# Optimization experiments

Measured on AMD Instinct MI355X. Metric: run time of the kernel, lower is better.

## Reference

```python
import jax, jax.numpy as jnp
import numpy as np

D = 1024
H = 16
F = 4096
EPS = 1e-6


def _layernorm(x, alpha, bias):
    # Faithful to torch: unbiased std (ddof=1), divide by (std + eps)
    mean = jnp.mean(x, axis=-1, keepdims=True)
    std = jnp.std(x, axis=-1, keepdims=True, ddof=1)
    return alpha * (x - mean) / (std + EPS) + bias


def setup_inputs() -> dict:
    key = jax.random.key(0)
    ks = jax.random.split(key, 12)
    B, S = 2, 2048
    s = 1.0 / np.sqrt(D)
    inp = {
        "x": jax.random.normal(ks[0], (B, S, D), jnp.float32),
        "mask": jnp.ones((B, 1, 1, S), jnp.int32),
        "wq": jax.random.normal(ks[1], (D, D), jnp.float32) * s,
        "bq": jnp.zeros((D,), jnp.float32),
        "wk": jax.random.normal(ks[2], (D, D), jnp.float32) * s,
        "bk": jnp.zeros((D,), jnp.float32),
        "wv": jax.random.normal(ks[3], (D, D), jnp.float32) * s,
        "bv": jnp.zeros((D,), jnp.float32),
        "wo": jax.random.normal(ks[4], (D, D), jnp.float32) * s,
        "bo": jnp.zeros((D,), jnp.float32),
        "ln1_a": jnp.ones((D,), jnp.float32),
        "ln1_b": jnp.zeros((D,), jnp.float32),
        "ln2_a": jnp.ones((D,), jnp.float32),
        "ln2_b": jnp.zeros((D,), jnp.float32),
        "w1": jax.random.normal(ks[5], (D, F), jnp.float32) * s,
        "b1": jnp.zeros((F,), jnp.float32),
        "w2": jax.random.normal(ks[6], (F, D), jnp.float32) * (1.0 / np.sqrt(F)),
        "b2": jnp.zeros((D,), jnp.float32),
    }
    return inp


def reference(x, mask, wq, bq, wk, bk, wv, bv, wo, bo,
              ln1_a, ln1_b, ln2_a, ln2_b, w1, b1, w2, b2):
    B, S, _ = x.shape
    dk = D // H
    # --- residual 1: pre-LN self-attention ---
    h = _layernorm(x, ln1_a, ln1_b)
    q = (h @ wq + bq).reshape(B, S, H, dk).transpose(0, 2, 1, 3)
    k = (h @ wk + bk).reshape(B, S, H, dk).transpose(0, 2, 1, 3)
    v = (h @ wv + bv).reshape(B, S, H, dk).transpose(0, 2, 1, 3)
    scores = jnp.einsum('bhqd,bhkd->bhqk', q, k) / jnp.sqrt(jnp.float32(dk))
    scores = jnp.where(mask == 0, jnp.float32(-1e9), scores)
    attn = jax.nn.softmax(scores, axis=-1)
    ctx = jnp.einsum('bhqk,bhkd->bhqd', attn, v)
    ctx = ctx.transpose(0, 2, 1, 3).reshape(B, S, D)
    x = x + (ctx @ wo + bo)
    # --- residual 2: pre-LN feed-forward ---
    h = _layernorm(x, ln2_a, ln2_b)
    ff = jax.nn.relu(h @ w1 + b1) @ w2 + b2
    return x + ff
```

## Files before the change

kernel.cpp:

```cpp
#include <hip/hip_runtime.h>
#include <hip/hip_bf16.h>

typedef __attribute__((ext_vector_type(8))) short bf16x8;
typedef __attribute__((ext_vector_type(4))) float f32x4;
typedef unsigned int uint32;

#define DMODEL 1024
#define SEQ    2048
#define NB     2
#define NH     16
#define HD     64
#define FDIM   4096
#define NTOK   (NB*SEQ)

__device__ __forceinline__ void async16(const void* g, void* s) {
    __builtin_amdgcn_global_load_lds((const __attribute__((address_space(1))) unsigned int*)g,
                                     (__attribute__((address_space(3))) unsigned int*)s,
                                     16, 0, 0);
}

__global__ __launch_bounds__(256) void transpose_cvt_k(const float* __restrict__ src,
                                                       __hip_bfloat16* __restrict__ dst,
                                                       int R, int C) {
    __shared__ __hip_bfloat16 tile[32][33];
    int tx = threadIdx.x, ty = threadIdx.y;
    int bx = blockIdx.x * 32, by = blockIdx.y * 32;
    for (int i = 0; i < 32; i += 8)
        tile[ty + i][tx] = __float2bfloat16(src[(size_t)(by + ty + i) * C + bx + tx]);
    __syncthreads();
    for (int i = 0; i < 32; i += 8)
        dst[(size_t)(bx + ty + i) * R + by + tx] = tile[tx][ty + i];
}

__global__ __launch_bounds__(256) void ln_kernel(const float* __restrict__ x,
                                                 const float* __restrict__ alpha,
                                                 const float* __restrict__ beta,
                                                 __hip_bfloat16* __restrict__ out) {
    const int row = blockIdx.x, tid = threadIdx.x;
    const size_t base = (size_t)row * DMODEL;
    float v[4];
    for (int e = 0; e < 4; ++e) v[e] = x[base + tid * 4 + e];
    float s1 = v[0] + v[1] + v[2] + v[3];
    float s2 = v[0]*v[0] + v[1]*v[1] + v[2]*v[2] + v[3]*v[3];
    for (int off = 32; off > 0; off >>= 1) {
        s1 += __shfl_down(s1, off);
        s2 += __shfl_down(s2, off);
    }
    __shared__ float red[8];
    int w = tid >> 6, lane = tid & 63;
    if (lane == 0) { red[w * 2] = s1; red[w * 2 + 1] = s2; }
    __syncthreads();
    if (tid == 0) {
        float a = 0.f, b = 0.f;
        for (int i = 0; i < 4; ++i) { a += red[2 * i]; b += red[2 * i + 1]; }
        red[0] = a; red[1] = b;
    }
    __syncthreads();
    s1 = red[0]; s2 = red[1];
    float mean = s1 * (1.0f / DMODEL);
    float var  = fmaxf((s2 - (float)DMODEL * mean * mean) * (1.0f / (DMODEL - 1)), 0.f);
    float inv  = 1.0f / (sqrtf(var) + 1e-6f);
    for (int e = 0; e < 4; ++e) {
        int c = tid * 4 + e;
        float y = alpha[c] * (v[e] - mean) * inv + beta[c];
        out[base + c] = __float2bfloat16(y);
    }
}

template <int EPI>
__global__ __launch_bounds__(256) void gemm_bt(const __hip_bfloat16* __restrict__ A,
                                               const __hip_bfloat16* __restrict__ Bt,
                                               const float* __restrict__ bias,
                                               const float* __restrict__ res,
                                               void* __restrict__ Cout,
                                               int M, int N, int K) {
    __shared__ alignas(16) __hip_bfloat16 As[2][128 * 32];
    __shared__ alignas(16) __hip_bfloat16 Bs[2][128 * 32];
    const int tid = threadIdx.x, l = tid & 63;
    const int w = tid >> 6;
    const int wm = w >> 1, wn = w & 1, quad = l >> 4, lc = l & 15;
    const int row0 = blockIdx.y * 128, col0 = blockIdx.x * 128;
    const int srow = 32 * w + (l >> 2), scol = (l & 3) * 8;

    f32x4 acc[4][4];
    for (int i = 0; i < 4; ++i)
        for (int j = 0; j < 4; ++j) acc[i][j] = (f32x4){0.f, 0.f, 0.f, 0.f};

    for (int c = 0; c < 2; ++c) {
        async16(A  + (size_t)(row0 + srow + 16 * c) * K + scol, (char*)&As[0][0] + w * 2048 + c * 1024);
        async16(Bt + (size_t)(col0 + srow + 16 * c) * K + scol, (char*)&Bs[0][0] + w * 2048 + c * 1024);
    }
    const int NKT = K / 32;
    for (int kt = 0; kt < NKT; ++kt) {
        const int cur = kt & 1;
        __syncthreads();
        if (kt + 1 < NKT) {
            const int k1 = (kt + 1) * 32;
            for (int c = 0; c < 2; ++c) {
                async16(A  + (size_t)(row0 + srow + 16 * c) * K + k1 + scol, (char*)&As[cur ^ 1][0] + w * 2048 + c * 1024);
                async16(Bt + (size_t)(col0 + srow + 16 * c) * K + k1 + scol, (char*)&Bs[cur ^ 1][0] + w * 2048 + c * 1024);
            }
        }
        bf16x8 af[4], bfr[4];
        for (int i = 0; i < 4; ++i) af[i]  = *(const bf16x8*)&As[cur][(64 * wm + 16 * i + lc) * 32 + quad * 8];
        for (int j = 0; j < 4; ++j) bfr[j] = *(const bf16x8*)&Bs[cur][(64 * wn + 16 * j + lc) * 32 + quad * 8];
        for (int i = 0; i < 4; ++i)
            for (int j = 0; j < 4; ++j)
                acc[i][j] = __builtin_amdgcn_mfma_f32_16x16x32_bf16(af[i], bfr[j], acc[i][j], 0, 0, 0);
    }

    __hip_bfloat16* Cb = (__hip_bfloat16*)Cout;
    float* Cf = (float*)Cout;
    for (int j = 0; j < 4; ++j) {
        int col = col0 + 64 * wn + 16 * j + lc;
        float bv = bias[col];
        for (int i = 0; i < 4; ++i) {
            int rbase = row0 + 64 * wm + 16 * i + quad * 4;
            for (int r = 0; r < 4; ++r) {
                size_t idx = (size_t)(rbase + r) * N + col;
                float vacc = acc[i][j][r] + bv;
                if (EPI == 0)      Cb[idx] = __float2bfloat16(vacc);
                else if (EPI == 1) Cb[idx] = __float2bfloat16(fmaxf(vacc, 0.f));
                else               Cf[idx] = vacc + res[idx];
            }
        }
    }
}

__global__ __launch_bounds__(256) void gemm_qkv(const __hip_bfloat16* __restrict__ A,
                                                const __hip_bfloat16* __restrict__ Bt,
                                                const float* __restrict__ bq,
                                                const float* __restrict__ bk,
                                                const float* __restrict__ bv,
                                                __hip_bfloat16* __restrict__ qout,
                                                __hip_bfloat16* __restrict__ kout,
                                                __hip_bfloat16* __restrict__ vTout) {
    const int K = DMODEL;
    __shared__ alignas(16) __hip_bfloat16 As[2][128 * 32];
    __shared__ alignas(16) __hip_bfloat16 Bs[2][128 * 32];
    const int tid = threadIdx.x, l = tid & 63;
    const int w = tid >> 6;
    const int wm = w >> 1, wn = w & 1, quad = l >> 4, lc = l & 15;
    const int row0 = blockIdx.y * 128, col0 = blockIdx.x * 128;
    const int srow = 32 * w + (l >> 2), scol = (l & 3) * 8;

    f32x4 acc[4][4];
    for (int i = 0; i < 4; ++i)
        for (int j = 0; j < 4; ++j) acc[i][j] = (f32x4){0.f, 0.f, 0.f, 0.f};

    for (int c = 0; c < 2; ++c) {
        async16(A  + (size_t)(row0 + srow + 16 * c) * K + scol, (char*)&As[0][0] + w * 2048 + c * 1024);
        async16(Bt + (size_t)(col0 + srow + 16 * c) * K + scol, (char*)&Bs[0][0] + w * 2048 + c * 1024);
    }
    const int NKT = K / 32;
    for (int kt = 0; kt < NKT; ++kt) {
        const int cur = kt & 1;
        __syncthreads();
        if (kt + 1 < NKT) {
            const int k1 = (kt + 1) * 32;
            for (int c = 0; c < 2; ++c) {
                async16(A  + (size_t)(row0 + srow + 16 * c) * K + k1 + scol, (char*)&As[cur ^ 1][0] + w * 2048 + c * 1024);
                async16(Bt + (size_t)(col0 + srow + 16 * c) * K + k1 + scol, (char*)&Bs[cur ^ 1][0] + w * 2048 + c * 1024);
            }
        }
        bf16x8 af[4], bfr[4];
        for (int i = 0; i < 4; ++i) af[i]  = *(const bf16x8*)&As[cur][(64 * wm + 16 * i + lc) * 32 + quad * 8];
        for (int j = 0; j < 4; ++j) bfr[j] = *(const bf16x8*)&Bs[cur][(64 * wn + 16 * j + lc) * 32 + quad * 8];
        for (int i = 0; i < 4; ++i)
            for (int j = 0; j < 4; ++j)
                acc[i][j] = __builtin_amdgcn_mfma_f32_16x16x32_bf16(af[i], bfr[j], acc[i][j], 0, 0, 0);
    }

    const int seg = col0 >> 10;
    const float* bias = (seg == 0) ? bq : (seg == 1) ? bk : bv;
    for (int j = 0; j < 4; ++j) {
        int col  = col0 + 64 * wn + 16 * j + lc;
        int colm = col & (DMODEL - 1);
        float bvx = bias[colm];
        for (int i = 0; i < 4; ++i) {
            int rbase = row0 + 64 * wm + 16 * i + quad * 4;
            for (int r = 0; r < 4; ++r) {
                int trow = rbase + r;
                float vacc = acc[i][j][r] + bvx;
                if (seg == 2) {
                    int bb = trow >> 11, s = trow & (SEQ - 1);
                    int hh = colm >> 6, d = colm & (HD - 1);
                    vTout[((size_t)(bb * NH + hh) * HD + d) * SEQ + s] = __float2bfloat16(vacc);
                } else {
                    __hip_bfloat16* dst = (seg == 0) ? qout : kout;
                    dst[(size_t)trow * DMODEL + colm] = __float2bfloat16(vacc);
                }
            }
        }
    }
}

__global__ __launch_bounds__(256) void attn_kernel(const __hip_bfloat16* __restrict__ q,
                                                   const __hip_bfloat16* __restrict__ k,
                                                   const __hip_bfloat16* __restrict__ vT,
                                                   const int* __restrict__ mask,
                                                   __hip_bfloat16* __restrict__ ctx) {
    const int qt = blockIdx.x, bh = blockIdx.y;
    const int b = bh >> 4;
    const int q0 = qt * 128;
    const int tid = threadIdx.x, w = tid >> 6, l = tid & 63, quad = l >> 4, lc = l & 15;

    __shared__ alignas(16) __hip_bfloat16 Kh[2][2][64 * 32];
    __shared__ alignas(16) __hip_bfloat16 Vh[2][2][64 * 32];
    __shared__ uint32 Ps32[4][16 * 33];

    const size_t base   = (size_t)b * SEQ * DMODEL + (size_t)(bh & 15) * HD;
    const size_t vtbase = (size_t)bh * HD * SEQ;

    bf16x8 qf[2][2];
    for (int s = 0; s < 2; ++s) {
        const __hip_bfloat16* qrow = &q[base + (size_t)(q0 + s * 64 + w * 16 + lc) * DMODEL];
        qf[s][0] = *(const bf16x8*)&qrow[quad * 8];
        qf[s][1] = *(const bf16x8*)&qrow[32 + quad * 8];
    }

    f32x4 o[2][4];
    for (int s = 0; s < 2; ++s)
        for (int dj = 0; dj < 4; ++dj) o[s][dj] = (f32x4){0.f, 0.f, 0.f, 0.f};
    float rsp[2][4] = {{0.f,0.f,0.f,0.f},{0.f,0.f,0.f,0.f}};

    const int lr = l >> 2, lc8 = (l & 3) * 8;

    for (int c = 0; c < 2; ++c) {
        const int W = w * 2 + c;
        const int rr = (W & 3) * 16 + lr, cc8 = (W >> 2) * 32 + lc8;
        async16(&k [base   + (size_t)rr * DMODEL + cc8], (char*)&Kh[0][0][0] + W * 1024);
        async16(&vT[vtbase + (size_t)rr * SEQ + cc8],    (char*)&Vh[0][0][0] + W * 1024);
    }

    const int NT = SEQ / 64;
    for (int kt = 0; kt < NT; ++kt) {
        const int k0 = kt * 64;
        const int cur = kt & 1;

        __syncthreads();
        if (kt + 1 < NT) {
            const int k1 = k0 + 64;
            for (int c = 0; c < 2; ++c) {
                const int W = w * 2 + c;
                const int rr = (W & 3) * 16 + lr, cc8 = (W >> 2) * 32 + lc8;
                async16(&k [base   + (size_t)(k1 + rr) * DMODEL + cc8], (char*)&Kh[cur ^ 1][0][0] + W * 1024);
                async16(&vT[vtbase + (size_t)rr * SEQ + k1 + cc8],      (char*)&Vh[cur ^ 1][0][0] + W * 1024);
            }
        }
        int mc[4];
        for (int jn = 0; jn < 4; ++jn) mc[jn] = mask[b * SEQ + k0 + jn * 16 + lc];

        bf16x8 kf0[4], kf1[4];
        for (int jn = 0; jn < 4; ++jn) {
            kf0[jn] = *(const bf16x8*)&Kh[cur][0][(jn * 16 + lc) * 32 + quad * 8];
            kf1[jn] = *(const bf16x8*)&Kh[cur][1][(jn * 16 + lc) * 32 + quad * 8];
        }
        f32x4 sa[2][4];
        for (int s = 0; s < 2; ++s)
            for (int jn = 0; jn < 4; ++jn) {
                f32x4 z = (f32x4){0.f, 0.f, 0.f, 0.f};
                z = __builtin_amdgcn_mfma_f32_16x16x32_bf16(qf[s][0], kf0[jn], z, 0, 0, 0);
                z = __builtin_amdgcn_mfma_f32_16x16x32_bf16(qf[s][1], kf1[jn], z, 0, 0, 0);
                sa[s][jn] = z;
            }

        bf16x8 vf0[4], vf1[4];
        for (int dj = 0; dj < 4; ++dj) {
            vf0[dj] = *(const bf16x8*)&Vh[cur][0][(dj * 16 + lc) * 32 + quad * 8];
            vf1[dj] = *(const bf16x8*)&Vh[cur][1][(dj * 16 + lc) * 32 + quad * 8];
        }

        for (int s = 0; s < 2; ++s) {
            float p[4][4];
            for (int jn = 0; jn < 4; ++jn)
                for (int r = 0; r < 4; ++r)
                    p[jn][r] = mc[jn] ? __expf(sa[s][jn][r] * 0.125f) : 0.f;
            for (int r = 0; r < 4; ++r)
                rsp[s][r] += (p[0][r] + p[1][r]) + (p[2][r] + p[3][r]);

            volatile unsigned short* psw = (volatile unsigned short*)&Ps32[w][0];
            for (int jn = 0; jn < 4; ++jn)
                for (int r = 0; r < 4; ++r) {
                    __hip_bfloat16 hb = __float2bfloat16(p[jn][r]);
                    psw[(quad * 4 + r) * 66 + jn * 16 + lc] = *(unsigned short*)&hb;
                }
            volatile uint32* plr = (volatile uint32*)&Ps32[w][0];
            union { uint32 u[4]; bf16x8 v8; } pf0, pf1;
            for (int j = 0; j < 4; ++j) {
                pf0.u[j] = plr[lc * 33 + quad * 4 + j];
                pf1.u[j] = plr[lc * 33 + 16 + quad * 4 + j];
            }
            for (int dj = 0; dj < 4; ++dj) {
                o[s][dj] = __builtin_amdgcn_mfma_f32_16x16x32_bf16(pf0.v8, vf0[dj], o[s][dj], 0, 0, 0);
                o[s][dj] = __builtin_amdgcn_mfma_f32_16x16x32_bf16(pf1.v8, vf1[dj], o[s][dj], 0, 0, 0);
            }
        }
    }

    for (int s = 0; s < 2; ++s) {
        for (int r = 0; r < 4; ++r) {
            float rs = rsp[s][r];
            for (int off = 1; off < 16; off <<= 1) rs += __shfl_xor(rs, off, 16);
            float linv = 1.0f / rs;
            int row = q0 + s * 64 + w * 16 + quad * 4 + r;
            for (int dj = 0; dj < 4; ++dj)
                ctx[base + (size_t)row * DMODEL + dj * 16 + lc] = __float2bfloat16(o[s][dj][r] * linv);
        }
    }
}

extern "C" void kernel_launch(void* const* d_in, const int* in_sizes, int n_in,
                              void* d_out, int out_size, void* d_ws, size_t ws_size,
                              hipStream_t stream) {
    const float* x    = (const float*)d_in[0];
    const int*   mask = (const int*)d_in[1];
    const float* wq = (const float*)d_in[2];
    const float* bq = (const float*)d_in[3];
    const float* wk = (const float*)d_in[4];
    const float* bk = (const float*)d_in[5];
    const float* wv = (const float*)d_in[6];
    const float* bv = (const float*)d_in[7];
    const float* wo = (const float*)d_in[8];
    const float* bo = (const float*)d_in[9];
    const float* ln1_a = (const float*)d_in[10];
    const float* ln1_b = (const float*)d_in[11];
    const float* ln2_a = (const float*)d_in[12];
    const float* ln2_b = (const float*)d_in[13];
    const float* w1 = (const float*)d_in[14];
    const float* b1 = (const float*)d_in[15];
    const float* w2 = (const float*)d_in[16];
    const float* b2 = (const float*)d_in[17];
    float* out = (float*)d_out;

    char* ws = (char*)d_ws;
    const size_t SZ_WT  = (size_t)DMODEL * DMODEL * 2;
    const size_t SZ_ACT = (size_t)NTOK * DMODEL * 2;
    const size_t SZ_WF  = (size_t)FDIM * DMODEL * 2;
    size_t off = 0;
    __hip_bfloat16* wqkvT = (__hip_bfloat16*)(ws + off); off += 3 * SZ_WT;
    __hip_bfloat16* woT   = (__hip_bfloat16*)(ws + off); off += SZ_WT;
    __hip_bfloat16* w1T   = (__hip_bfloat16*)(ws + off); off += SZ_WF;
    __hip_bfloat16* w2T   = (__hip_bfloat16*)(ws + off); off += SZ_WF;
    __hip_bfloat16* h1    = (__hip_bfloat16*)(ws + off); off += SZ_ACT;
    __hip_bfloat16* qb    = (__hip_bfloat16*)(ws + off); off += SZ_ACT;
    __hip_bfloat16* kb    = (__hip_bfloat16*)(ws + off); off += SZ_ACT;
    __hip_bfloat16* vTb   = (__hip_bfloat16*)(ws + off); off += SZ_ACT;
    __hip_bfloat16* ctx   = (__hip_bfloat16*)(ws + off); off += SZ_ACT;
    float*          x1    = (float*)(ws + off);          off += (size_t)NTOK * DMODEL * 4;
    __hip_bfloat16* h2    = (__hip_bfloat16*)(ws + off); off += SZ_ACT;
    __hip_bfloat16* ff1   = h1;

    dim3 tb(32, 8);
    transpose_cvt_k<<<dim3(32, 32), tb, 0, stream>>>(wq, wqkvT,                   DMODEL, DMODEL);
    transpose_cvt_k<<<dim3(32, 32), tb, 0, stream>>>(wk, wqkvT + 1024 * DMODEL,   DMODEL, DMODEL);
    transpose_cvt_k<<<dim3(32, 32), tb, 0, stream>>>(wv, wqkvT + 2048 * DMODEL,   DMODEL, DMODEL);
    transpose_cvt_k<<<dim3(32, 32), tb, 0, stream>>>(wo, woT, DMODEL, DMODEL);
    transpose_cvt_k<<<dim3(128, 32), tb, 0, stream>>>(w1, w1T, DMODEL, FDIM);
    transpose_cvt_k<<<dim3(32, 128), tb, 0, stream>>>(w2, w2T, FDIM, DMODEL);

    ln_kernel<<<NTOK, 256, 0, stream>>>(x, ln1_a, ln1_b, h1);

    gemm_qkv<<<dim3(3 * DMODEL / 128, NTOK / 128), 256, 0, stream>>>(h1, wqkvT, bq, bk, bv, qb, kb, vTb);

    attn_kernel<<<dim3(SEQ / 128, NB * NH), 256, 0, stream>>>(qb, kb, vTb, mask, ctx);

    gemm_bt<2><<<dim3(DMODEL / 128, NTOK / 128), 256, 0, stream>>>(ctx, woT, bo, x, x1, NTOK, DMODEL, DMODEL);

    ln_kernel<<<NTOK, 256, 0, stream>>>(x1, ln2_a, ln2_b, h2);

    gemm_bt<1><<<dim3(FDIM / 128, NTOK / 128), 256, 0, stream>>>(h2, w1T, b1, nullptr, ff1, NTOK, FDIM, DMODEL);
    gemm_bt<2><<<dim3(DMODEL / 128, NTOK / 128), 256, 0, stream>>>(ff1, w2T, b2, x1, out, NTOK, DMODEL, FDIM);
}
```

Before: 453.8 us.

## Swizzle K/V LDS tiles and pass P via lane shuffles instead of LDS

The attention kernel now computes S transposed (K as the A operand), so each lane holds the scores for one query column across four key rows. It packs the probabilities to bf16 and rearranges them into the PV MFMA operand layout with two xor-shuffles, which removes the per-wave LDS scratch round trip for P. K/V tiles are written to and read from LDS with an XOR swizzle to reduce bank conflicts, mask loads are vectorized to int4, and s_setprio is raised around the MFMA blocks. The row-sum reduction is reworked to match the new layout, which adds shuffle and select work and depends on the lane-mapping being correct.

```diff
diff --git a/kernel.cpp b/kernel.cpp
--- a/kernel.cpp
+++ b/kernel.cpp
@@ -207,7 +207,6 @@
 
     __shared__ alignas(16) __hip_bfloat16 Kh[2][2][64 * 32];
     __shared__ alignas(16) __hip_bfloat16 Vh[2][2][64 * 32];
-    __shared__ uint32 Ps32[4][16 * 33];
 
     const size_t base   = (size_t)b * SEQ * DMODEL + (size_t)(bh & 15) * HD;
     const size_t vtbase = (size_t)bh * HD * SEQ;
@@ -222,13 +221,16 @@
     f32x4 o[2][4];
     for (int s = 0; s < 2; ++s)
         for (int dj = 0; dj < 4; ++dj) o[s][dj] = (f32x4){0.f, 0.f, 0.f, 0.f};
-    float rsp[2][4] = {{0.f,0.f,0.f,0.f},{0.f,0.f,0.f,0.f}};
-
-    const int lr = l >> 2, lc8 = (l & 3) * 8;
+    float rsp2[2] = {0.f, 0.f};
+
+    const int lr  = l >> 2, cb = l & 3;
+    const int cbsw = ((cb ^ ((lr >> 1) & 3))) * 8;
+    const int rsw  = (lc >> 1) & 3;
+    const int b1v = (l >> 5) & 1, b0v = (l >> 4) & 1;
 
     for (int c = 0; c < 2; ++c) {
         const int W = w * 2 + c;
-        const int rr = (W & 3) * 16 + lr, cc8 = (W >> 2) * 32 + lc8;
+        const int rr = (W & 3) * 16 + lr, cc8 = (W >> 2) * 32 + cbsw;
         async16(&k [base   + (size_t)rr * DMODEL + cc8], (char*)&Kh[0][0][0] + W * 1024);
         async16(&vT[vtbase + (size_t)rr * SEQ + cc8],    (char*)&Vh[0][0][0] + W * 1024);
     }
@@ -243,66 +245,91 @@
             const int k1 = k0 + 64;
             for (int c = 0; c < 2; ++c) {
                 const int W = w * 2 + c;
-                const int rr = (W & 3) * 16 + lr, cc8 = (W >> 2) * 32 + lc8;
+                const int rr = (W & 3) * 16 + lr, cc8 = (W >> 2) * 32 + cbsw;
                 async16(&k [base   + (size_t)(k1 + rr) * DMODEL + cc8], (char*)&Kh[cur ^ 1][0][0] + W * 1024);
                 async16(&vT[vtbase + (size_t)rr * SEQ + k1 + cc8],      (char*)&Vh[cur ^ 1][0][0] + W * 1024);
             }
         }
-        int mc[4];
-        for (int jn = 0; jn < 4; ++jn) mc[jn] = mask[b * SEQ + k0 + jn * 16 + lc];
+        int4 mc[4];
+        for (int jn = 0; jn < 4; ++jn)
+            mc[jn] = *(const int4*)&mask[b * SEQ + k0 + jn * 16 + quad * 4];
 
         bf16x8 kf0[4], kf1[4];
         for (int jn = 0; jn < 4; ++jn) {
-            kf0[jn] = *(const bf16x8*)&Kh[cur][0][(jn * 16 + lc) * 32 + quad * 8];
-            kf1[jn] = *(const bf16x8*)&Kh[cur][1][(jn * 16 + lc) * 32 + quad * 8];
-        }
-        f32x4 sa[2][4];
-        for (int s = 0; s < 2; ++s)
+            kf0[jn] = *(const bf16x8*)&Kh[cur][0][(jn * 16 + lc) * 32 + (quad ^ rsw) * 8];
+            kf1[jn] = *(const bf16x8*)&Kh[cur][1][(jn * 16 + lc) * 32 + (quad ^ rsw) * 8];
+        }
+        bf16x8 vf0[4], vf1[4];
+        for (int dj = 0; dj < 4; ++dj) {
+            vf0[dj] = *(const bf16x8*)&Vh[cur][0][(dj * 16 + lc) * 32 + (quad ^ rsw) * 8];
+            vf1[dj] = *(const bf16x8*)&Vh[cur][1][(dj * 16 + lc) * 32 + (quad ^ rsw) * 8];
+        }
+
+        for (int s = 0; s < 2; ++s) {
+            f32x4 sa[4];
+            __builtin_amdgcn_s_setprio(1);
             for (int jn = 0; jn < 4; ++jn) {
                 f32x4 z = (f32x4){0.f, 0.f, 0.f, 0.f};
-                z = __builtin_amdgcn_mfma_f32_16x16x32_bf16(qf[s][0], kf0[jn], z, 0, 0, 0);
-                z = __builtin_amdgcn_mfma_f32_16x16x32_bf16(qf[s][1], kf1[jn], z, 0, 0, 0);
-                sa[s][jn] = z;
-            }
-
-        bf16x8 vf0[4], vf1[4];
-        for (int dj = 0; dj < 4; ++dj) {
-            vf0[dj] = *(const bf16x8*)&Vh[cur][0][(dj * 16 + lc) * 32 + quad * 8];
-            vf1[dj] = *(const bf16x8*)&Vh[cur][1][(dj * 16 + lc) * 32 + quad * 8];
-        }
-
-        for (int s = 0; s < 2; ++s) {
-            float p[4][4];
-            for (int jn = 0; jn < 4; ++jn)
-                for (int r = 0; r < 4; ++r)
-                    p[jn][r] = mc[jn] ? __expf(sa[s][jn][r] * 0.125f) : 0.f;
-            for (int r = 0; r < 4; ++r)
-                rsp[s][r] += (p[0][r] + p[1][r]) + (p[2][r] + p[3][r]);
-
-            volatile unsigned short* psw = (volatile unsigned short*)&Ps32[w][0];
-            for (int jn = 0; jn < 4; ++jn)
-                for (int r = 0; r < 4; ++r) {
-                    __hip_bfloat16 hb = __float2bfloat16(p[jn][r]);
-                    psw[(quad * 4 + r) * 66 + jn * 16 + lc] = *(unsigned short*)&hb;
-                }
-            volatile uint32* plr = (volatile uint32*)&Ps32[w][0];
+                z = __builtin_amdgcn_mfma_f32_16x16x32_bf16(kf0[jn], qf[s][0], z, 0, 0, 0);
+                z = __builtin_amdgcn_mfma_f32_16x16x32_bf16(kf1[jn], qf[s][1], z, 0, 0, 0);
+                sa[jn] = z;
+            }
+            __builtin_amdgcn_s_setprio(0);
+
+            uint32 wd[4][2];
+            float accs = 0.f;
+            for (int jn = 0; jn < 4; ++jn) {
+                float p0 = mc[jn].x ? __expf(sa[jn][0] * 0.125f) : 0.f;
+                float p1 = mc[jn].y ? __expf(sa[jn][1] * 0.125f) : 0.f;
+                float p2 = mc[jn].z ? __expf(sa[jn][2] * 0.125f) : 0.f;
+                float p3 = mc[jn].w ? __expf(sa[jn][3] * 0.125f) : 0.f;
+                accs += (p0 + p1) + (p2 + p3);
+                __hip_bfloat16 h0 = __float2bfloat16(p0), h1 = __float2bfloat16(p1);
+                __hip_bfloat16 h2 = __float2bfloat16(p2), h3 = __float2bfloat16(p3);
+                wd[jn][0] = (uint32)*(unsigned short*)&h0 | ((uint32)*(unsigned short*)&h1 << 16);
+                wd[jn][1] = (uint32)*(unsigned short*)&h2 | ((uint32)*(unsigned short*)&h3 << 16);
+            }
+            rsp2[s] += accs;
+
+            uint32 send1[4], kept[4];
+            send1[0] = b1v ? wd[0][0] : wd[1][0];  kept[0] = b1v ? wd[1][0] : wd[0][0];
+            send1[1] = b1v ? wd[0][1] : wd[1][1];  kept[1] = b1v ? wd[1][1] : wd[0][1];
+            send1[2] = b1v ? wd[2][0] : wd[3][0];  kept[2] = b1v ? wd[3][0] : wd[2][0];
+            send1[3] = b1v ? wd[2][1] : wd[3][1];  kept[3] = b1v ? wd[3][1] : wd[2][1];
+            uint32 recv1[4];
+            for (int t = 0; t < 4; ++t) recv1[t] = (uint32)__shfl_xor((int)send1[t], 32);
+            uint32 send2[4], stay[4];
+            for (int t = 0; t < 4; ++t) {
+                send2[t] = (b1v == b0v) ? recv1[t] : kept[t];
+                stay[t]  = (b1v == b0v) ? kept[t]  : recv1[t];
+            }
+            uint32 recv2[4];
+            for (int t = 0; t < 4; ++t) recv2[t] = (uint32)__shfl_xor((int)send2[t], 16);
+            uint32 G0[4], G1[4];
+            for (int t = 0; t < 4; ++t) {
+                G0[t] = b0v ? recv2[t] : stay[t];
+                G1[t] = b0v ? stay[t]  : recv2[t];
+            }
             union { uint32 u[4]; bf16x8 v8; } pf0, pf1;
-            for (int j = 0; j < 4; ++j) {
-                pf0.u[j] = plr[lc * 33 + quad * 4 + j];
-                pf1.u[j] = plr[lc * 33 + 16 + quad * 4 + j];
-            }
+            pf0.u[0] = G0[0]; pf0.u[1] = G0[1]; pf0.u[2] = G1[0]; pf0.u[3] = G1[1];
+            pf1.u[0] = G0[2]; pf1.u[1] = G0[3]; pf1.u[2] = G1[2]; pf1.u[3] = G1[3];
+
+            __builtin_amdgcn_s_setprio(1);
             for (int dj = 0; dj < 4; ++dj) {
                 o[s][dj] = __builtin_amdgcn_mfma_f32_16x16x32_bf16(pf0.v8, vf0[dj], o[s][dj], 0, 0, 0);
                 o[s][dj] = __builtin_amdgcn_mfma_f32_16x16x32_bf16(pf1.v8, vf1[dj], o[s][dj], 0, 0, 0);
             }
+            __builtin_amdgcn_s_setprio(0);
         }
     }
 
     for (int s = 0; s < 2; ++s) {
+        float rs = rsp2[s];
+        rs += __shfl_xor(rs, 16);
+        rs += __shfl_xor(rs, 32);
         for (int r = 0; r < 4; ++r) {
-            float rs = rsp[s][r];
-            for (int off = 1; off < 16; off <<= 1) rs += __shfl_xor(rs, off, 16);
-            float linv = 1.0f / rs;
+            float rq = __shfl(rs, (l & 48) | (quad * 4 + r));
+            float linv = 1.0f / rq;
             int row = q0 + s * 64 + w * 16 + quad * 4 + r;
             for (int dj = 0; dj < 4; ++dj)
                 ctx[base + (size_t)row * DMODEL + dj * 16 + lc] = __float2bfloat16(o[s][dj][r] * linv);
```

Measured after the change: 428.1 us. 1.06x faster.
